# Performance work log

Measured on AMD Instinct MI355X. Metric: run time of the kernel, lower is better.

The kernel has to match this reference:

```python
import jax, jax.numpy as jnp
import numpy as np

DIM = 96
SHIFT_SIZE = 3
EPS = 1e-5


def conv1x1(x, w, b):
    # x: [B,C,H,W], w: [O,C], b: [O]
    return jnp.einsum('bchw,oc->bohw', x, w) + b[None, :, None, None]


def group_norm1(x, gamma, beta):
    # GroupNorm with 1 group: normalize over (C,H,W) per sample
    mean = jnp.mean(x, axis=(1, 2, 3), keepdims=True)
    var = jnp.var(x, axis=(1, 2, 3), keepdims=True)
    xn = (x - mean) * jax.lax.rsqrt(var + EPS)
    return xn * gamma[None, :, None, None] + beta[None, :, None, None]


def axial_shift(x, shift_size, axis, sign=1):
    # pad -> chunk channels -> roll each chunk -> cat -> narrow (zero-fill shift)
    B, C, H, W = x.shape
    p = shift_size // 2
    xp = jnp.pad(x, ((0, 0), (0, 0), (p, p), (p, p)))
    chunks = jnp.split(xp, shift_size, axis=1)
    rolled = [jnp.roll(c, sign * s, axis=axis) for c, s in zip(chunks, range(-p, p + 1))]
    xc = jnp.concatenate(rolled, axis=1)
    return xc[:, :, p:p + H, p:p + W]


def setup_inputs() -> dict:
    key = jax.random.key(0)
    ks = jax.random.split(key, 13)
    B, C, H, W = 4, DIM, 256, 256
    s = 1.0 / np.sqrt(C)
    inp = {
        'x': jax.random.normal(ks[0], (B, C, H, W), jnp.float32),
        'w1': jax.random.uniform(ks[1], (C, C), jnp.float32, -s, s),
        'b1': jax.random.uniform(ks[2], (C,), jnp.float32, -s, s),
        'w21': jax.random.uniform(ks[3], (C, C), jnp.float32, -s, s),
        'b21': jax.random.uniform(ks[4], (C,), jnp.float32, -s, s),
        'w22': jax.random.uniform(ks[5], (C, C), jnp.float32, -s, s),
        'b22': jax.random.uniform(ks[6], (C,), jnp.float32, -s, s),
        'w3': jax.random.uniform(ks[7], (C, C), jnp.float32, -s, s),
        'b3': jax.random.uniform(ks[8], (C,), jnp.float32, -s, s),
        'gn1_w': jnp.ones((C,), jnp.float32),
        'gn1_b': jnp.zeros((C,), jnp.float32),
        'gn2_w': jnp.ones((C,), jnp.float32),
        'gn2_b': jnp.zeros((C,), jnp.float32),
    }
    return inp


def reference(x, w1, b1, w21, b21, w22, b22, w3, b3, gn1_w, gn1_b, gn2_w, gn2_b):
    gelu = lambda t: jax.nn.gelu(t, approximate=False)  # torch nn.GELU default (erf)
    x = gelu(group_norm1(conv1x1(x, w1, b1), gn1_w, gn1_b))
    x_lr = axial_shift(x, SHIFT_SIZE, axis=3)
    x_l_diag = axial_shift(x_lr, SHIFT_SIZE, axis=2)
    x_td = axial_shift(x, SHIFT_SIZE, axis=2)
    x_r_diag = axial_shift(x_td, SHIFT_SIZE, axis=3, sign=-1)
    out = (gelu(conv1x1(x_lr, w21, b21)) + gelu(conv1x1(x_l_diag, w21, b21))
           + gelu(conv1x1(x_td, w22, b22)) + gelu(conv1x1(x_r_diag, w22, b22)))
    out = group_norm1(out, gn2_w, gn2_b)
    return conv1x1(out, w3, b3)
```

## Files before the change

### kernel.cpp

```cpp
#include <hip/hip_runtime.h>
#include <hip/hip_bf16.h>
#include <math.h>


#define B_ 4
#define C_ 96
#define H_ 256
#define W_ 256
#define NPIX (H_ * W_)
#define GN_N ((float)(C_ * NPIX))
#define CPAD 104

#define HT 8
#define WT 16
#define HHT (HT + 2)
#define HWT (WT + 2)
#define HALO_PX (HHT * HWT)
#define GR_PX 12
#define ROW_GR (HWT * GR_PX)
#define TOT_GR (HHT * ROW_GR)

typedef __attribute__((ext_vector_type(4))) float f32x4;
typedef __attribute__((ext_vector_type(8))) short short8;
typedef __attribute__((ext_vector_type(2))) unsigned int uint2v;

__device__ __forceinline__ unsigned short f2bf(float v) {
    unsigned int u = __float_as_uint(v);
    unsigned int r = (u + 0x7FFFu + ((u >> 16) & 1u)) >> 16;
    return (unsigned short)r;
}
__device__ __forceinline__ float bf2f(unsigned short u) {
    return __uint_as_float(((unsigned int)u) << 16);
}

__device__ __forceinline__ float gelu_f(float v) {
    float t = fmaf(v * v, 0.1029433f, 2.3021178f);
    float e = __builtin_amdgcn_exp2f(v * t);
    float r = __builtin_amdgcn_rcpf(e + 1.0f);
    return v - v * r;
}

__device__ __forceinline__ float waveReduceSum(float v) {
#pragma unroll
    for (int off = 32; off > 0; off >>= 1) v += __shfl_down(v, off);
    return v;
}

__device__ __forceinline__ f32x4 mfma16(short8 a, short8 b, f32x4 c) {
    return __builtin_amdgcn_mfma_f32_16x16x32_bf16(a, b, c, 0, 0, 0);
}

__global__ void k0_prep(const float* __restrict__ w1, const float* __restrict__ w21,
                        const float* __restrict__ w22, const float* __restrict__ w3,
                        unsigned short* __restrict__ wb, float* __restrict__ stats) {
    int t = blockIdx.x * 256 + threadIdx.x;
    if (blockIdx.x == 0 && threadIdx.x < 16) stats[threadIdx.x] = 0.f;
    if (t >= 4 * C_ * C_) return;
    int m = t / (C_ * C_);
    int r = t - m * (C_ * C_);
    const float* src = (m == 0) ? w1 : (m == 1) ? w21 : (m == 2) ? w22 : w3;
    wb[t] = f2bf(src[r]);
}

__global__ __launch_bounds__(256, 3) void k1_conv1(
    const float* __restrict__ x, const unsigned short* __restrict__ w1b,
    const float* __restrict__ b1, unsigned short* __restrict__ ap,
    float* __restrict__ stats) {
    __shared__ unsigned short xs[256 * CPAD];
    __shared__ float red[8];
    int tid = threadIdx.x;
    int b = blockIdx.x >> 8;
    int h = blockIdx.x & 255;
    int pix0 = h << 8;
    size_t xbase = (size_t)b * C_ * NPIX + pix0 + tid;
    int lb = tid * CPAD;
#pragma unroll
    for (int c0 = 0; c0 < C_; c0 += 8) {
        short8 pk;
#pragma unroll
        for (int j = 0; j < 8; ++j)
            pk[j] = (short)f2bf(x[xbase + (size_t)(c0 + j) * NPIX]);
        *reinterpret_cast<short8*>(&xs[lb + c0]) = pk;
    }
    __syncthreads();
    int l = tid & 63, wv = tid >> 6;
    int bx = l & 15, q = l >> 4, cl = q * 8;
    short8 bfr[4][3];
#pragma unroll
    for (int nf = 0; nf < 4; ++nf) {
        int p = (4 * wv + nf) * 16 + bx;
#pragma unroll
        for (int kb = 0; kb < 3; ++kb)
            bfr[nf][kb] = *reinterpret_cast<const short8*>(&xs[p * CPAD + kb * 32 + cl]);
    }
    unsigned int* xsu = reinterpret_cast<unsigned int*>(xs);
    float ls = 0.f, lsq = 0.f;
    for (int mt = 0; mt < 6; ++mt) {
        int m0 = mt * 16;
        const unsigned short* wp = w1b + (m0 + bx) * C_ + cl;
        short8 af[3];
#pragma unroll
        for (int kb = 0; kb < 3; ++kb)
            af[kb] = *reinterpret_cast<const short8*>(wp + kb * 32);
        f32x4 acc[4];
#pragma unroll
        for (int nf = 0; nf < 4; ++nf) acc[nf] = (f32x4){0.f, 0.f, 0.f, 0.f};
#pragma unroll
        for (int nf = 0; nf < 4; ++nf)
#pragma unroll
            for (int kb = 0; kb < 3; ++kb)
                acc[nf] = mfma16(af[kb], bfr[nf][kb], acc[nf]);
        int o = m0 + q * 4;
        float b0 = b1[o], b1v = b1[o + 1], b2v = b1[o + 2], b3v = b1[o + 3];
#pragma unroll
        for (int nf = 0; nf < 4; ++nf) {
            int p = (4 * wv + nf) * 16 + bx;
            float y0 = acc[nf][0] + b0, y1v = acc[nf][1] + b1v;
            float y2 = acc[nf][2] + b2v, y3 = acc[nf][3] + b3v;
            ls += y0 + y1v + y2 + y3;
            lsq += y0 * y0 + y1v * y1v + y2 * y2 + y3 * y3;
            xsu[p * (CPAD / 2) + (o >> 1)] =
                (unsigned int)f2bf(y0) | ((unsigned int)f2bf(y1v) << 16);
            xsu[p * (CPAD / 2) + (o >> 1) + 1] =
                (unsigned int)f2bf(y2) | ((unsigned int)f2bf(y3) << 16);
        }
    }
    __syncthreads();
    size_t abase = (size_t)(b * NPIX + pix0 + tid) * C_;
#pragma unroll
    for (int c0 = 0; c0 < C_; c0 += 8)
        *reinterpret_cast<short8*>(&ap[abase + c0]) =
            *reinterpret_cast<short8*>(&xs[tid * CPAD + c0]);
    ls = waveReduceSum(ls);
    lsq = waveReduceSum(lsq);
    if (l == 0) { red[wv] = ls; red[4 + wv] = lsq; }
    __syncthreads();
    if (tid == 0) {
        atomicAdd(&stats[b], red[0] + red[1] + red[2] + red[3]);
        atomicAdd(&stats[4 + b], red[4] + red[5] + red[6] + red[7]);
    }
}

__global__ void k2_fin(float* stats, int so, int dof) {
    int t = threadIdx.x;
    if (t < 4) {
        float mean = stats[so + t] / GN_N;
        float var = stats[so + 4 + t] / GN_N - mean * mean;
        stats[dof + t] = mean;
        stats[dof + 4 + t] = rsqrtf(var + 1e-5f);
    }
}

__global__ __launch_bounds__(256, 4) void k3_main(
    const unsigned short* __restrict__ ap,
    const unsigned short* __restrict__ w21b, const float* __restrict__ b21,
    const unsigned short* __restrict__ w22b, const float* __restrict__ b22,
    const float* __restrict__ gn1w, const float* __restrict__ gn1b,
    unsigned short* __restrict__ zb, float* __restrict__ stats) {
    __shared__ unsigned short as_t[HALO_PX * CPAD];
    __shared__ float red[8];
    __shared__ float scs[C_], offs[C_];
    int tid = threadIdx.x;
    int wseg = blockIdx.x & 15;
    int hseg = (blockIdx.x >> 4) & 31;
    int b = blockIdx.x >> 9;
    int l = tid & 63, wv = tid >> 6;
    int h0 = hseg * HT, w0 = wseg * WT;
    float m1 = stats[16 + b], r1 = stats[20 + b];
    if (tid < C_) {
        float sc = r1 * gn1w[tid];
        scs[tid] = sc;
        offs[tid] = gn1b[tid] - m1 * sc;
    }
    __syncthreads();
    for (int g = tid; g < TOT_GR; g += 256) {
        int row = g / ROW_GR;
        int rem = g - row * ROW_GR;
        int p = rem / GR_PX;
        int cgr = rem - p * GR_PX;
        int hh = h0 - 1 + row, ww = w0 - 1 + p;
        bool valid = ((unsigned)hh < (unsigned)H_) && ((unsigned)ww < (unsigned)W_);
        int hc = valid ? hh : 0, wc = valid ? ww : 0;
        short8 raw = *reinterpret_cast<const short8*>(
            &ap[(size_t)(b * NPIX + hc * W_ + wc) * C_ + cgr * 8]);
        short8 pk;
#pragma unroll
        for (int j = 0; j < 8; ++j) {
            int c = cgr * 8 + j;
            float f = bf2f((unsigned short)raw[j]);
            float gv = gelu_f(fmaf(f, scs[c], offs[c]));
            pk[j] = valid ? (short)f2bf(gv) : (short)0;
        }
        *reinterpret_cast<short8*>(&as_t[(row * HWT + p) * CPAD + cgr * 8]) = pk;
    }
    __syncthreads();
    int bx = l & 15, q = l >> 4, cl = q * 8;
    int Xb = (bx + 1) * CPAD + cl;
#define FR(R, dx, kb) (*reinterpret_cast<const short8*>( \
        &as_t[((R)*HWT + (dx)) * CPAD + Xb + (kb)*32]))
    float ls = 0.f, lsq = 0.f;
#pragma unroll
    for (int nf = 0; nf < 2; ++nf) {
        int r = 2 * wv + nf;
        short8 f0a = FR(r + 1, 1, 0), f0b = FR(r + 2, 1, 0);
        short8 f0c = FR(r + 2, 0, 0), f0d = FR(r + 2, -1, 0);
        short8 fC = FR(r + 1, 0, 1);
        short8 f2a = FR(r + 1, -1, 2), f2b = FR(r, -1, 2);
        short8 f2c = FR(r, 0, 2), f2d = FR(r, 1, 2);
        size_t zpix = (size_t)(b * NPIX + (h0 + r) * W_ + w0 + bx) * C_;
        for (int mt = 0; mt < 6; ++mt) {
            int m0 = mt * 16;
            const unsigned short* wpa = w21b + (m0 + bx) * C_ + cl;
            const unsigned short* wpb = w22b + (m0 + bx) * C_ + cl;
            short8 aA0 = *reinterpret_cast<const short8*>(wpa);
            short8 aA1 = *reinterpret_cast<const short8*>(wpa + 32);
            short8 aA2 = *reinterpret_cast<const short8*>(wpa + 64);
            short8 aB0 = *reinterpret_cast<const short8*>(wpb);
            short8 aB1 = *reinterpret_cast<const short8*>(wpb + 32);
            short8 aB2 = *reinterpret_cast<const short8*>(wpb + 64);
            const f32x4 bb1 = *reinterpret_cast<const f32x4*>(&b21[m0 + q * 4]);
            const f32x4 bb2 = *reinterpret_cast<const f32x4*>(&b22[m0 + q * 4]);
            f32x4 a0 = bb1, a1 = bb1, a2 = bb2, a3 = bb2;
            a0 = mfma16(aA0, f0a, a0);
            a1 = mfma16(aA0, f0b, a1);
            a2 = mfma16(aB0, f0c, a2);
            a3 = mfma16(aB0, f0d, a3);
            a0 = mfma16(aA1, fC, a0);
            a1 = mfma16(aA1, fC, a1);
            a2 = mfma16(aB1, fC, a2);
            a3 = mfma16(aB1, fC, a3);
            a0 = mfma16(aA2, f2a, a0);
            a1 = mfma16(aA2, f2b, a1);
            a2 = mfma16(aB2, f2c, a2);
            a3 = mfma16(aB2, f2d, a3);
            float zv[4];
#pragma unroll
            for (int rg = 0; rg < 4; ++rg) {
                float z0 = gelu_f(a0[rg]) + gelu_f(a1[rg]) +
                           gelu_f(a2[rg]) + gelu_f(a3[rg]);
                zv[rg] = z0;
                ls += z0;
                lsq += z0 * z0;
            }
            uint2v pk;
            pk.x = (unsigned int)f2bf(zv[0]) | ((unsigned int)f2bf(zv[1]) << 16);
            pk.y = (unsigned int)f2bf(zv[2]) | ((unsigned int)f2bf(zv[3]) << 16);
            *reinterpret_cast<uint2v*>(&zb[zpix + m0 + q * 4]) = pk;
        }
    }
#undef FR
    ls = waveReduceSum(ls);
    lsq = waveReduceSum(lsq);
    if (l == 0) { red[wv] = ls; red[4 + wv] = lsq; }
    __syncthreads();
    if (tid == 0) {
        atomicAdd(&stats[8 + b], red[0] + red[1] + red[2] + red[3]);
        atomicAdd(&stats[12 + b], red[4] + red[5] + red[6] + red[7]);
    }
}

__global__ void k4b_fold(const float* __restrict__ w3, const float* __restrict__ b3,
                         const float* __restrict__ gn2w, const float* __restrict__ gn2b,
                         const float* __restrict__ stats,
                         unsigned short* __restrict__ w3p, float* __restrict__ b3p) {
    int b = blockIdx.x;
    int o = threadIdx.x;
    float mean = stats[8 + b] / GN_N;
    float var = stats[12 + b] / GN_N - mean * mean;
    float r2 = rsqrtf(var + 1e-5f);
    float acc = 0.f;
    for (int c = 0; c < C_; ++c) {
        float sc = r2 * gn2w[c];
        float off = gn2b[c] - mean * sc;
        float wv = w3[o * C_ + c];
        acc = fmaf(wv, off, acc);
        w3p[((size_t)b * C_ + o) * C_ + c] = f2bf(wv * sc);
    }
    b3p[b * C_ + o] = acc + b3[o];
}

__global__ __launch_bounds__(256, 3) void k5_conv3(
    const unsigned short* __restrict__ zb,
    const unsigned short* __restrict__ w3p, const float* __restrict__ b3p,
    float* __restrict__ out) {
    __shared__ unsigned short zs[256 * CPAD];
    int tid = threadIdx.x;
    int b = blockIdx.x >> 8;
    int pix0 = (blockIdx.x & 255) << 8;
    {
        const short8* src = reinterpret_cast<const short8*>(
            &zb[(size_t)(b * NPIX + pix0 + tid) * C_]);
        int lb = tid * CPAD;
#pragma unroll
        for (int i = 0; i < 12; ++i)
            *reinterpret_cast<short8*>(&zs[lb + i * 8]) = src[i];
    }
    __syncthreads();
    int l = tid & 63, wv = tid >> 6;
    int bx = l & 15, q = l >> 4, cl = q * 8;
    short8 bfr[4][3];
#pragma unroll
    for (int nf = 0; nf < 4; ++nf) {
        int p = (4 * wv + nf) * 16 + bx;
#pragma unroll
        for (int kb = 0; kb < 3; ++kb)
            bfr[nf][kb] = *reinterpret_cast<const short8*>(&zs[p * CPAD + kb * 32 + cl]);
    }
    const unsigned short* wbase = w3p + (size_t)b * C_ * C_;
    const float* bb = b3p + b * C_;
    for (int mt = 0; mt < 6; ++mt) {
        int m0 = mt * 16;
        const unsigned short* wp = wbase + (m0 + bx) * C_ + cl;
        short8 af0 = *reinterpret_cast<const short8*>(wp);
        short8 af1 = *reinterpret_cast<const short8*>(wp + 32);
        short8 af2 = *reinterpret_cast<const short8*>(wp + 64);
        f32x4 acc[4];
#pragma unroll
        for (int nf = 0; nf < 4; ++nf) acc[nf] = (f32x4){0.f, 0.f, 0.f, 0.f};
#pragma unroll
        for (int nf = 0; nf < 4; ++nf) {
            acc[nf] = mfma16(af0, bfr[nf][0], acc[nf]);
            acc[nf] = mfma16(af1, bfr[nf][1], acc[nf]);
            acc[nf] = mfma16(af2, bfr[nf][2], acc[nf]);
        }
        int o = m0 + q * 4;
        float b0 = bb[o], b1v = bb[o + 1], b2v = bb[o + 2], b3v = bb[o + 3];
#pragma unroll
        for (int nf = 0; nf < 4; ++nf) {
            int p = pix0 + (4 * wv + nf) * 16 + bx;
            size_t ob0 = (size_t)(b * C_ + o) * NPIX + p;
            out[ob0] = acc[nf][0] + b0;
            out[ob0 + NPIX] = acc[nf][1] + b1v;
            out[ob0 + 2 * NPIX] = acc[nf][2] + b2v;
            out[ob0 + 3 * NPIX] = acc[nf][3] + b3v;
        }
    }
}

extern "C" void kernel_launch(void* const* d_in, const int* in_sizes, int n_in,
                              void* d_out, int out_size, void* d_ws, size_t ws_size,
                              hipStream_t stream) {
    const float* x = (const float*)d_in[0];
    const float* w1 = (const float*)d_in[1];
    const float* b1 = (const float*)d_in[2];
    const float* w21 = (const float*)d_in[3];
    const float* b21 = (const float*)d_in[4];
    const float* w22 = (const float*)d_in[5];
    const float* b22 = (const float*)d_in[6];
    const float* w3 = (const float*)d_in[7];
    const float* b3 = (const float*)d_in[8];
    const float* gn1w = (const float*)d_in[9];
    const float* gn1b = (const float*)d_in[10];
    const float* gn2w = (const float*)d_in[11];
    const float* gn2b = (const float*)d_in[12];
    float* out = (float*)d_out;
    char* ws = (char*)d_ws;

    const size_t NB = (size_t)B_ * NPIX * C_ * sizeof(unsigned short);
    unsigned short* ap = (unsigned short*)ws;
    unsigned short* zb = (unsigned short*)(ws + NB);
    float* stats = (float*)(ws + 2 * NB);
    unsigned short* wb = (unsigned short*)(ws + 2 * NB + 128);
    unsigned short* w1b = wb;
    unsigned short* w21b = wb + C_ * C_;
    unsigned short* w22b = wb + 2 * C_ * C_;
    unsigned short* w3p = wb + 4 * C_ * C_;
    float* b3p = (float*)(w3p + B_ * C_ * C_);

    hipLaunchKernelGGL(k0_prep, dim3(144), dim3(256), 0, stream,
                       w1, w21, w22, w3, wb, stats);
    hipLaunchKernelGGL(k1_conv1, dim3(1024), dim3(256), 0, stream, x, w1b, b1, ap, stats);
    hipLaunchKernelGGL(k2_fin, dim3(1), dim3(64), 0, stream, stats, 0, 16);
    hipLaunchKernelGGL(k3_main, dim3(2048), dim3(256), 0, stream,
                       ap, w21b, b21, w22b, b22, gn1w, gn1b, zb, stats);
    hipLaunchKernelGGL(k4b_fold, dim3(B_), dim3(C_), 0, stream,
                       w3, b3, gn2w, gn2b, stats, w3p, b3p);
    hipLaunchKernelGGL(k5_conv3, dim3(1024), dim3(256), 0, stream,
                       zb, w3p, b3p, out);
}
```

Baseline: 176.2 us.

## Halve conv tiles, double k3 threads, use packed bf16 conversion instruction

```diff
diff --git a/kernel.cpp b/kernel.cpp
--- a/kernel.cpp
+++ b/kernel.cpp
@@ -23,14 +23,20 @@
 typedef __attribute__((ext_vector_type(4))) float f32x4;
 typedef __attribute__((ext_vector_type(8))) short short8;
 typedef __attribute__((ext_vector_type(2))) unsigned int uint2v;
-
+typedef __attribute__((ext_vector_type(4))) unsigned int uint4v;
+
+__device__ __forceinline__ float bf2f(unsigned short u) {
+    return __uint_as_float(((unsigned int)u) << 16);
+}
 __device__ __forceinline__ unsigned short f2bf(float v) {
     unsigned int u = __float_as_uint(v);
     unsigned int r = (u + 0x7FFFu + ((u >> 16) & 1u)) >> 16;
     return (unsigned short)r;
 }
-__device__ __forceinline__ float bf2f(unsigned short u) {
-    return __uint_as_float(((unsigned int)u) << 16);
+__device__ __forceinline__ unsigned int cvtpk(float lo, float hi) {
+    unsigned int r;
+    asm("v_cvt_pk_bf16_f32 %0, %1, %2" : "=v"(r) : "v"(lo), "v"(hi));
+    return r;
 }
 
 __device__ __forceinline__ float gelu_f(float v) {
@@ -62,33 +68,37 @@
     wb[t] = f2bf(src[r]);
 }
 
-__global__ __launch_bounds__(256, 3) void k1_conv1(
+__global__ __launch_bounds__(256, 6) void k1_conv1(
     const float* __restrict__ x, const unsigned short* __restrict__ w1b,
     const float* __restrict__ b1, unsigned short* __restrict__ ap,
     float* __restrict__ stats) {
-    __shared__ unsigned short xs[256 * CPAD];
+    __shared__ unsigned short xs[128 * CPAD];
     __shared__ float red[8];
     int tid = threadIdx.x;
-    int b = blockIdx.x >> 8;
-    int h = blockIdx.x & 255;
-    int pix0 = h << 8;
-    size_t xbase = (size_t)b * C_ * NPIX + pix0 + tid;
-    int lb = tid * CPAD;
-#pragma unroll
-    for (int c0 = 0; c0 < C_; c0 += 8) {
-        short8 pk;
-#pragma unroll
-        for (int j = 0; j < 8; ++j)
-            pk[j] = (short)f2bf(x[xbase + (size_t)(c0 + j) * NPIX]);
-        *reinterpret_cast<short8*>(&xs[lb + c0]) = pk;
+    int b = blockIdx.x >> 9;
+    int pix0 = (blockIdx.x & 511) << 7;
+    int pix = tid & 127, half = tid >> 7;
+    size_t xbase = (size_t)b * C_ * NPIX + pix0 + pix;
+    {
+        int lb = pix * CPAD + half * 48;
+#pragma unroll
+        for (int cc = 0; cc < 48; cc += 8) {
+            int c = half * 48 + cc;
+            float f[8];
+#pragma unroll
+            for (int j = 0; j < 8; ++j) f[j] = x[xbase + (size_t)(c + j) * NPIX];
+            uint4v pk = {cvtpk(f[0], f[1]), cvtpk(f[2], f[3]),
+                         cvtpk(f[4], f[5]), cvtpk(f[6], f[7])};
+            *reinterpret_cast<uint4v*>(&xs[lb + cc]) = pk;
+        }
     }
     __syncthreads();
     int l = tid & 63, wv = tid >> 6;
     int bx = l & 15, q = l >> 4, cl = q * 8;
-    short8 bfr[4][3];
-#pragma unroll
-    for (int nf = 0; nf < 4; ++nf) {
-        int p = (4 * wv + nf) * 16 + bx;
+    short8 bfr[2][3];
+#pragma unroll
+    for (int nf = 0; nf < 2; ++nf) {
+        int p = (2 * wv + nf) * 16 + bx;
 #pragma unroll
         for (int kb = 0; kb < 3; ++kb)
             bfr[nf][kb] = *reinterpret_cast<const short8*>(&xs[p * CPAD + kb * 32 + cl]);
@@ -102,35 +112,36 @@
 #pragma unroll
         for (int kb = 0; kb < 3; ++kb)
             af[kb] = *reinterpret_cast<const short8*>(wp + kb * 32);
-        f32x4 acc[4];
-#pragma unroll
-        for (int nf = 0; nf < 4; ++nf) acc[nf] = (f32x4){0.f, 0.f, 0.f, 0.f};
-#pragma unroll
-        for (int nf = 0; nf < 4; ++nf)
+        f32x4 acc[2];
+#pragma unroll
+        for (int nf = 0; nf < 2; ++nf) acc[nf] = (f32x4){0.f, 0.f, 0.f, 0.f};
+#pragma unroll
+        for (int nf = 0; nf < 2; ++nf)
 #pragma unroll
             for (int kb = 0; kb < 3; ++kb)
                 acc[nf] = mfma16(af[kb], bfr[nf][kb], acc[nf]);
         int o = m0 + q * 4;
         float b0 = b1[o], b1v = b1[o + 1], b2v = b1[o + 2], b3v = b1[o + 3];
 #pragma unroll
-        for (int nf = 0; nf < 4; ++nf) {
-            int p = (4 * wv + nf) * 16 + bx;
+        for (int nf = 0; nf < 2; ++nf) {
+            int p = (2 * wv + nf) * 16 + bx;
             float y0 = acc[nf][0] + b0, y1v = acc[nf][1] + b1v;
             float y2 = acc[nf][2] + b2v, y3 = acc[nf][3] + b3v;
             ls += y0 + y1v + y2 + y3;
             lsq += y0 * y0 + y1v * y1v + y2 * y2 + y3 * y3;
-            xsu[p * (CPAD / 2) + (o >> 1)] =
-                (unsigned int)f2bf(y0) | ((unsigned int)f2bf(y1v) << 16);
-            xsu[p * (CPAD / 2) + (o >> 1) + 1] =
-                (unsigned int)f2bf(y2) | ((unsigned int)f2bf(y3) << 16);
-        }
-    }
-    __syncthreads();
-    size_t abase = (size_t)(b * NPIX + pix0 + tid) * C_;
-#pragma unroll
-    for (int c0 = 0; c0 < C_; c0 += 8)
-        *reinterpret_cast<short8*>(&ap[abase + c0]) =
-            *reinterpret_cast<short8*>(&xs[tid * CPAD + c0]);
+            xsu[p * (CPAD / 2) + (o >> 1)] = cvtpk(y0, y1v);
+            xsu[p * (CPAD / 2) + (o >> 1) + 1] = cvtpk(y2, y3);
+        }
+    }
+    __syncthreads();
+    {
+        size_t abase = (size_t)(b * NPIX + pix0 + pix) * C_ + half * 48;
+        int lb = pix * CPAD + half * 48;
+#pragma unroll
+        for (int cc = 0; cc < 48; cc += 8)
+            *reinterpret_cast<short8*>(&ap[abase + cc]) =
+                *reinterpret_cast<short8*>(&xs[lb + cc]);
+    }
     ls = waveReduceSum(ls);
     lsq = waveReduceSum(lsq);
     if (l == 0) { red[wv] = ls; red[4 + wv] = lsq; }
@@ -151,14 +162,14 @@
     }
 }
 
-__global__ __launch_bounds__(256, 4) void k3_main(
+__global__ __launch_bounds__(512, 8) void k3_main(
     const unsigned short* __restrict__ ap,
     const unsigned short* __restrict__ w21b, const float* __restrict__ b21,
     const unsigned short* __restrict__ w22b, const float* __restrict__ b22,
     const float* __restrict__ gn1w, const float* __restrict__ gn1b,
     unsigned short* __restrict__ zb, float* __restrict__ stats) {
     __shared__ unsigned short as_t[HALO_PX * CPAD];
-    __shared__ float red[8];
+    __shared__ float red[16];
     __shared__ float scs[C_], offs[C_];
     int tid = threadIdx.x;
     int wseg = blockIdx.x & 15;
@@ -173,25 +184,28 @@
         offs[tid] = gn1b[tid] - m1 * sc;
     }
     __syncthreads();
-    for (int g = tid; g < TOT_GR; g += 256) {
+    for (int g = tid; g < TOT_GR; g += 512) {
         int row = g / ROW_GR;
         int rem = g - row * ROW_GR;
         int p = rem / GR_PX;
         int cgr = rem - p * GR_PX;
         int hh = h0 - 1 + row, ww = w0 - 1 + p;
-        bool valid = ((unsigned)hh < (unsigned)H_) && ((unsigned)ww < (unsigned)W_);
-        int hc = valid ? hh : 0, wc = valid ? ww : 0;
-        short8 raw = *reinterpret_cast<const short8*>(
-            &ap[(size_t)(b * NPIX + hc * W_ + wc) * C_ + cgr * 8]);
-        short8 pk;
-#pragma unroll
-        for (int j = 0; j < 8; ++j) {
-            int c = cgr * 8 + j;
-            float f = bf2f((unsigned short)raw[j]);
-            float gv = gelu_f(fmaf(f, scs[c], offs[c]));
-            pk[j] = valid ? (short)f2bf(gv) : (short)0;
-        }
-        *reinterpret_cast<short8*>(&as_t[(row * HWT + p) * CPAD + cgr * 8]) = pk;
+        unsigned short* dst = &as_t[(row * HWT + p) * CPAD + cgr * 8];
+        if (((unsigned)hh < (unsigned)H_) && ((unsigned)ww < (unsigned)W_)) {
+            short8 raw = *reinterpret_cast<const short8*>(
+                &ap[(size_t)(b * NPIX + hh * W_ + ww) * C_ + cgr * 8]);
+            float gv[8];
+#pragma unroll
+            for (int j = 0; j < 8; ++j) {
+                int c = cgr * 8 + j;
+                gv[j] = gelu_f(fmaf(bf2f((unsigned short)raw[j]), scs[c], offs[c]));
+            }
+            uint4v pk = {cvtpk(gv[0], gv[1]), cvtpk(gv[2], gv[3]),
+                         cvtpk(gv[4], gv[5]), cvtpk(gv[6], gv[7])};
+            *reinterpret_cast<uint4v*>(dst) = pk;
+        } else {
+            *reinterpret_cast<uint4v*>(dst) = (uint4v){0, 0, 0, 0};
+        }
     }
     __syncthreads();
     int bx = l & 15, q = l >> 4, cl = q * 8;
@@ -199,9 +213,8 @@
 #define FR(R, dx, kb) (*reinterpret_cast<const short8*>( \
         &as_t[((R)*HWT + (dx)) * CPAD + Xb + (kb)*32]))
     float ls = 0.f, lsq = 0.f;
-#pragma unroll
-    for (int nf = 0; nf < 2; ++nf) {
-        int r = 2 * wv + nf;
+    {
+        int r = wv;
         short8 f0a = FR(r + 1, 1, 0), f0b = FR(r + 2, 1, 0);
         short8 f0c = FR(r + 2, 0, 0), f0d = FR(r + 2, -1, 0);
         short8 fC = FR(r + 1, 0, 1);
@@ -243,19 +256,22 @@
                 lsq += z0 * z0;
             }
             uint2v pk;
-            pk.x = (unsigned int)f2bf(zv[0]) | ((unsigned int)f2bf(zv[1]) << 16);
-            pk.y = (unsigned int)f2bf(zv[2]) | ((unsigned int)f2bf(zv[3]) << 16);
+            pk.x = cvtpk(zv[0], zv[1]);
+            pk.y = cvtpk(zv[2], zv[3]);
             *reinterpret_cast<uint2v*>(&zb[zpix + m0 + q * 4]) = pk;
         }
     }
 #undef FR
     ls = waveReduceSum(ls);
     lsq = waveReduceSum(lsq);
-    if (l == 0) { red[wv] = ls; red[4 + wv] = lsq; }
+    if (l == 0) { red[wv] = ls; red[8 + wv] = lsq; }
     __syncthreads();
     if (tid == 0) {
-        atomicAdd(&stats[8 + b], red[0] + red[1] + red[2] + red[3]);
-        atomicAdd(&stats[12 + b], red[4] + red[5] + red[6] + red[7]);
+        float s0 = 0.f, s1 = 0.f;
+#pragma unroll
+        for (int i = 0; i < 8; ++i) { s0 += red[i]; s1 += red[8 + i]; }
+        atomicAdd(&stats[8 + b], s0);
+        atomicAdd(&stats[12 + b], s1);
     }
 }
 
@@ -279,29 +295,30 @@
     b3p[b * C_ + o] = acc + b3[o];
 }
 
-__global__ __launch_bounds__(256, 3) void k5_conv3(
+__global__ __launch_bounds__(256, 6) void k5_conv3(
     const unsigned short* __restrict__ zb,
     const unsigned short* __restrict__ w3p, const float* __restrict__ b3p,
     float* __restrict__ out) {
-    __shared__ unsigned short zs[256 * CPAD];
+    __shared__ unsigned short zs[128 * CPAD];
     int tid = threadIdx.x;
-    int b = blockIdx.x >> 8;
-    int pix0 = (blockIdx.x & 255) << 8;
+    int b = blockIdx.x >> 9;
+    int pix0 = (blockIdx.x & 511) << 7;
+    int pix = tid & 127, half = tid >> 7;
     {
         const short8* src = reinterpret_cast<const short8*>(
-            &zb[(size_t)(b * NPIX + pix0 + tid) * C_]);
-        int lb = tid * CPAD;
-#pragma unroll
-        for (int i = 0; i < 12; ++i)
+            &zb[(size_t)(b * NPIX + pix0 + pix) * C_ + half * 48]);
+        int lb = pix * CPAD + half * 48;
+#pragma unroll
+        for (int i = 0; i < 6; ++i)
             *reinterpret_cast<short8*>(&zs[lb + i * 8]) = src[i];
     }
     __syncthreads();
     int l = tid & 63, wv = tid >> 6;
     int bx = l & 15, q = l >> 4, cl = q * 8;
-    short8 bfr[4][3];
-#pragma unroll
-    for (int nf = 0; nf < 4; ++nf) {
-        int p = (4 * wv + nf) * 16 + bx;
+    short8 bfr[2][3];
+#pragma unroll
+    for (int nf = 0; nf < 2; ++nf) {
+        int p = (2 * wv + nf) * 16 + bx;
 #pragma unroll
         for (int kb = 0; kb < 3; ++kb)
             bfr[nf][kb] = *reinterpret_cast<const short8*>(&zs[p * CPAD + kb * 32 + cl]);
@@ -314,11 +331,11 @@
         short8 af0 = *reinterpret_cast<const short8*>(wp);
         short8 af1 = *reinterpret_cast<const short8*>(wp + 32);
         short8 af2 = *reinterpret_cast<const short8*>(wp + 64);
-        f32x4 acc[4];
-#pragma unroll
-        for (int nf = 0; nf < 4; ++nf) acc[nf] = (f32x4){0.f, 0.f, 0.f, 0.f};
-#pragma unroll
-        for (int nf = 0; nf < 4; ++nf) {
+        f32x4 acc[2];
+#pragma unroll
+        for (int nf = 0; nf < 2; ++nf) acc[nf] = (f32x4){0.f, 0.f, 0.f, 0.f};
+#pragma unroll
+        for (int nf = 0; nf < 2; ++nf) {
             acc[nf] = mfma16(af0, bfr[nf][0], acc[nf]);
             acc[nf] = mfma16(af1, bfr[nf][1], acc[nf]);
             acc[nf] = mfma16(af2, bfr[nf][2], acc[nf]);
@@ -326,8 +343,8 @@
         int o = m0 + q * 4;
         float b0 = bb[o], b1v = bb[o + 1], b2v = bb[o + 2], b3v = bb[o + 3];
 #pragma unroll
-        for (int nf = 0; nf < 4; ++nf) {
-            int p = pix0 + (4 * wv + nf) * 16 + bx;
+        for (int nf = 0; nf < 2; ++nf) {
+            int p = pix0 + (2 * wv + nf) * 16 + bx;
             size_t ob0 = (size_t)(b * C_ + o) * NPIX + p;
             out[ob0] = acc[nf][0] + b0;
             out[ob0 + NPIX] = acc[nf][1] + b1v;
@@ -369,12 +386,12 @@
 
     hipLaunchKernelGGL(k0_prep, dim3(144), dim3(256), 0, stream,
                        w1, w21, w22, w3, wb, stats);
-    hipLaunchKernelGGL(k1_conv1, dim3(1024), dim3(256), 0, stream, x, w1b, b1, ap, stats);
+    hipLaunchKernelGGL(k1_conv1, dim3(2048), dim3(256), 0, stream, x, w1b, b1, ap, stats);
     hipLaunchKernelGGL(k2_fin, dim3(1), dim3(64), 0, stream, stats, 0, 16);
-    hipLaunchKernelGGL(k3_main, dim3(2048), dim3(256), 0, stream,
+    hipLaunchKernelGGL(k3_main, dim3(2048), dim3(512), 0, stream,
                        ap, w21b, b21, w22b, b22, gn1w, gn1b, zb, stats);
     hipLaunchKernelGGL(k4b_fold, dim3(B_), dim3(C_), 0, stream,
                        w3, b3, gn2w, gn2b, stats, w3p, b3p);
-    hipLaunchKernelGGL(k5_conv3, dim3(1024), dim3(256), 0, stream,
+    hipLaunchKernelGGL(k5_conv3, dim3(2048), dim3(256), 0, stream,
                        zb, w3p, b3p, out);
 }
```

Result: slower. 260.2 us (+47.7%).
